# Kernel tuning notes

Hardware: AMD Instinct MI355X
Metric: run time of the kernel (lower is better)

## Reference

```python
import jax, jax.numpy as jnp
import numpy as np

N_NODES = 50000
N_EDGES = 640000
IN_FEATS = 128
HID = 128


def setup_inputs() -> dict:
    key = jax.random.key(0)
    ks = jax.random.split(key, 8)
    x = jax.random.normal(ks[0], (N_NODES, IN_FEATS), dtype=jnp.float32)
    src = jax.random.randint(ks[1], (N_EDGES,), 0, N_NODES, dtype=jnp.int32)
    dst = jax.random.randint(ks[2], (N_EDGES,), 0, N_NODES, dtype=jnp.int32)
    s1 = 1.0 / np.sqrt(IN_FEATS)
    s2 = 1.0 / np.sqrt(HID)
    W1 = jax.random.normal(ks[3], (IN_FEATS, HID), dtype=jnp.float32) * s1
    b1 = jnp.zeros((HID,), dtype=jnp.float32)
    W2 = jax.random.normal(ks[4], (HID, HID), dtype=jnp.float32) * s2
    b2 = jnp.zeros((HID,), dtype=jnp.float32)
    Wr = jax.random.normal(ks[5], (HID, 2), dtype=jnp.float32) * s2
    br = jnp.zeros((2,), dtype=jnp.float32)
    return {"x": x, "src": src, "dst": dst, "W1": W1, "b1": b1,
            "W2": W2, "b2": b2, "Wr": Wr, "br": br}


def _degree_norm(idx, n):
    # D^{-1/2}, with 0 for zero-degree nodes (DGL sets inf -> 0)
    deg = jax.ops.segment_sum(jnp.ones(idx.shape[0], jnp.float32), idx, num_segments=n)
    return jnp.where(deg > 0, jax.lax.rsqrt(jnp.maximum(deg, 1.0)), 0.0)


def _graph_conv(h, W, b, src, dst, norm_out, norm_in, n):
    # DGL GraphConv, norm='both': out = D_in^{-1/2} A D_out^{-1/2} (h W) + b
    hW = (h * norm_out[:, None]) @ W          # [N, hid]
    agg = jax.ops.segment_sum(hW[src], dst, num_segments=n)  # gather+scatter over edges
    return agg * norm_in[:, None] + b


def reference(x, src, dst, W1, b1, W2, b2, Wr, br):
    n = x.shape[0]
    norm_out = _degree_norm(src, n)  # source-side out-degree norm
    norm_in = _degree_norm(dst, n)   # dest-side in-degree norm
    h = jax.nn.relu(_graph_conv(x, W1, b1, src, dst, norm_out, norm_in, n))
    h = jax.nn.relu(_graph_conv(h, W2, b2, src, dst, norm_out, norm_in, n))
    hg = jnp.mean(h, axis=0, keepdims=True)  # [1, hid]
    return hg @ Wr + br                      # [1, 2]
```

## Files before the change

### kernel.cpp

```cpp
#include <hip/hip_runtime.h>
#include <hip/hip_bf16.h>

#define FEAT 128
#define RBITS 13
#define RSIZE 8192
#define NCHUNK 32

typedef __attribute__((ext_vector_type(8))) short short8;
typedef __attribute__((ext_vector_type(4))) short short4v;
typedef __attribute__((ext_vector_type(4))) float f32x4;

__device__ __forceinline__ ushort f2bf(float f) {
    union { float f; unsigned u; } v; v.f = f;
    unsigned u = v.u;
    unsigned r = 0x7fffu + ((u >> 16) & 1u);
    return (ushort)((u + r) >> 16);
}
__device__ __forceinline__ float bf2f(short s) {
    union { unsigned u; float f; } v;
    v.u = ((unsigned)(ushort)s) << 16;
    return v.f;
}

__global__ __launch_bounds__(256)
void hist_kernel(const int* __restrict__ src, const int* __restrict__ dst,
                 unsigned* __restrict__ partial, int E, int CS)
{
    __shared__ unsigned hist[RSIZE];
    const int c = blockIdx.x, p = blockIdx.y, job = blockIdx.z;
    const int* __restrict__ idx = job ? dst : src;
    for (int r = threadIdx.x; r < RSIZE; r += 256) hist[r] = 0;
    __syncthreads();
    const int e0 = c * CS, e1 = min(E, e0 + CS);
    const int eA = e0 + ((e1 - e0) & ~3);
    for (int e = e0 + threadIdx.x * 4; e + 4 <= e1; e += 1024) {
        int4 v = *(const int4*)(idx + e);
        if ((v.x >> RBITS) == p) atomicAdd(&hist[v.x & (RSIZE - 1)], 1u);
        if ((v.y >> RBITS) == p) atomicAdd(&hist[v.y & (RSIZE - 1)], 1u);
        if ((v.z >> RBITS) == p) atomicAdd(&hist[v.z & (RSIZE - 1)], 1u);
        if ((v.w >> RBITS) == p) atomicAdd(&hist[v.w & (RSIZE - 1)], 1u);
    }
    for (int e = eA + threadIdx.x; e < e1; e += 256) {
        int v = idx[e];
        if ((v >> RBITS) == p) atomicAdd(&hist[v & (RSIZE - 1)], 1u);
    }
    __syncthreads();
    unsigned* outp = partial +
        (((size_t)job * gridDim.y + p) * NCHUNK + c) * RSIZE;
    for (int r = threadIdx.x; r < RSIZE; r += 256) outp[r] = hist[r];
}

__global__ __launch_bounds__(256)
void merge_kernel(const unsigned* __restrict__ partialOut, unsigned* __restrict__ partialIn,
                  int* __restrict__ cntIn, float* __restrict__ normOut,
                  float* __restrict__ normIn, int* __restrict__ blockSums, int N)
{
    __shared__ int sh[256];
    const int n = blockIdx.x * 256 + threadIdx.x;
    unsigned off = 0;
    if (n < N) {
        const int p = n >> RBITS, r = n & (RSIZE - 1);
        const size_t base = (size_t)p * NCHUNK * RSIZE + r;
        unsigned so = 0;
#pragma unroll 8
        for (int c = 0; c < NCHUNK; ++c) so += partialOut[base + (size_t)c * RSIZE];
#pragma unroll 8
        for (int c = 0; c < NCHUNK; ++c) {
            size_t i = base + (size_t)c * RSIZE;
            unsigned t = partialIn[i];
            partialIn[i] = off;
            off += t;
        }
        cntIn[n]   = (int)off;
        normIn[n]  = off ? rsqrtf((float)off) : 0.0f;
        normOut[n] = so  ? rsqrtf((float)so)  : 0.0f;
    }
    sh[threadIdx.x] = (int)off;
    __syncthreads();
    for (int o = 128; o > 0; o >>= 1) {
        if (threadIdx.x < o) sh[threadIdx.x] += sh[threadIdx.x + o];
        __syncthreads();
    }
    if (threadIdx.x == 0) blockSums[blockIdx.x] = sh[0];
}

__global__ __launch_bounds__(256)
void rowstart_kernel(const int* __restrict__ cntIn, const int* __restrict__ blockSums,
                     int* __restrict__ rowStart, int N, int NB, int E)
{
    __shared__ int bs[256];
    __shared__ int bse[256];
    __shared__ int sh[256];
    const int t = threadIdx.x;
    int bv = (t < NB) ? blockSums[t] : 0;
    bs[t] = bv;
    __syncthreads();
    for (int off = 1; off < 256; off <<= 1) {
        int u = (t >= off) ? bs[t - off] : 0;
        __syncthreads();
        bs[t] += u;
        __syncthreads();
    }
    bse[t] = bs[t] - bv;
    __syncthreads();

    const int i = blockIdx.x * 256 + t;
    int v = (i < N) ? cntIn[i] : 0;
    sh[t] = v;
    __syncthreads();
    for (int off = 1; off < 256; off <<= 1) {
        int u = (t >= off) ? sh[t - off] : 0;
        __syncthreads();
        sh[t] += u;
        __syncthreads();
    }
    if (i < N) rowStart[i] = bse[blockIdx.x] + sh[t] - v;
    if (blockIdx.x == 0 && t == 0) rowStart[N] = E;
}

__global__ __launch_bounds__(256)
void fill_kernel(const int* __restrict__ src, const int* __restrict__ dst,
                 const int* __restrict__ rowStart, const unsigned* __restrict__ chunkOff,
                 int* __restrict__ csrSrc, int N, int E, int CS)
{
    __shared__ unsigned cursor[RSIZE];
    const int c = blockIdx.x, p = blockIdx.y;
    const unsigned* co = chunkOff + ((size_t)p * NCHUNK + c) * RSIZE;
    for (int r = threadIdx.x; r < RSIZE; r += 256) {
        int n = (p << RBITS) + r;
        cursor[r] = (n < N) ? (unsigned)rowStart[n] + co[r] : 0u;
    }
    __syncthreads();
    const int e0 = c * CS, e1 = min(E, e0 + CS);
    const int eA = e0 + ((e1 - e0) & ~3);
    for (int e = e0 + threadIdx.x * 4; e + 4 <= e1; e += 1024) {
        int4 d = *(const int4*)(dst + e);
        if ((d.x >> RBITS) == p) { unsigned q = atomicAdd(&cursor[d.x & (RSIZE - 1)], 1u); csrSrc[q] = src[e]; }
        if ((d.y >> RBITS) == p) { unsigned q = atomicAdd(&cursor[d.y & (RSIZE - 1)], 1u); csrSrc[q] = src[e + 1]; }
        if ((d.z >> RBITS) == p) { unsigned q = atomicAdd(&cursor[d.z & (RSIZE - 1)], 1u); csrSrc[q] = src[e + 2]; }
        if ((d.w >> RBITS) == p) { unsigned q = atomicAdd(&cursor[d.w & (RSIZE - 1)], 1u); csrSrc[q] = src[e + 3]; }
    }
    for (int e = eA + threadIdx.x; e < e1; e += 256) {
        int d = dst[e];
        if ((d >> RBITS) == p) { unsigned q = atomicAdd(&cursor[d & (RSIZE - 1)], 1u); csrSrc[q] = src[e]; }
    }
}

__global__ __launch_bounds__(256)
void gemm_mfma_kernel(const float* __restrict__ Ain, const float* __restrict__ W,
                      const float* __restrict__ scale, ushort* __restrict__ C,
                      int M, int nStrips)
{
    __shared__ ushort WTAs[128 * 132];
    __shared__ float  sScale[64];
    ushort* WT = WTAs;
    ushort* As = WTAs;

    const int tid  = threadIdx.x;
    const int wv   = tid >> 6;
    const int lane = tid & 63;
    const int rowHalf = wv >> 1;
    const int colHalf = wv & 1;
    const int l15  = lane & 15;
    const int quad = lane >> 4;

    for (int it = 0; it < 16; ++it) {
        int fid = tid + (it << 8);
        int k   = fid >> 5;
        int c4  = (fid & 31) << 2;
        float4 w = *(const float4*)(W + (size_t)k * FEAT + c4);
        WT[(c4 + 0) * 132 + k] = f2bf(w.x);
        WT[(c4 + 1) * 132 + k] = f2bf(w.y);
        WT[(c4 + 2) * 132 + k] = f2bf(w.z);
        WT[(c4 + 3) * 132 + k] = f2bf(w.w);
    }
    __syncthreads();

    short8 bfrag[4][4];
#pragma unroll
    for (int ct = 0; ct < 4; ++ct) {
        int col = colHalf * 64 + ct * 16 + l15;
#pragma unroll
        for (int kst = 0; kst < 4; ++kst) {
            int k = kst * 32 + quad * 8;
            short4v lo = *(const short4v*)&WT[col * 132 + k];
            short4v hi = *(const short4v*)&WT[col * 132 + k + 4];
            bfrag[ct][kst] = __builtin_shufflevector(lo, hi, 0, 1, 2, 3, 4, 5, 6, 7);
        }
    }

    for (int s = blockIdx.x; s < nStrips; s += gridDim.x) {
        const int row0 = s << 6;
        __syncthreads();

#pragma unroll
        for (int it = 0; it < 4; ++it) {
            int fid = tid + (it << 8);
            int r   = fid >> 4;
            int seg = (fid & 15) << 3;
            int grow = row0 + r;
            short4v lo = {0, 0, 0, 0}, hi = {0, 0, 0, 0};
            if (grow < M) {
                const float* pa = Ain + (size_t)grow * FEAT + seg;
                float4 u0 = *(const float4*)(pa);
                float4 u1 = *(const float4*)(pa + 4);
                lo[0] = (short)f2bf(u0.x); lo[1] = (short)f2bf(u0.y);
                lo[2] = (short)f2bf(u0.z); lo[3] = (short)f2bf(u0.w);
                hi[0] = (short)f2bf(u1.x); hi[1] = (short)f2bf(u1.y);
                hi[2] = (short)f2bf(u1.z); hi[3] = (short)f2bf(u1.w);
            }
            *(short4v*)&As[r * 132 + seg]     = lo;
            *(short4v*)&As[r * 132 + seg + 4] = hi;
        }
        if (tid < 64) {
            int grow = row0 + tid;
            sScale[tid] = (grow < M) ? scale[grow] : 0.0f;
        }
        __syncthreads();

        f32x4 acc[2][4] = {};
#pragma unroll
        for (int kst = 0; kst < 4; ++kst) {
            int k = kst * 32 + quad * 8;
            short8 af[2];
#pragma unroll
            for (int rt = 0; rt < 2; ++rt) {
                int row = rowHalf * 32 + rt * 16 + l15;
                short4v lo = *(const short4v*)&As[row * 132 + k];
                short4v hi = *(const short4v*)&As[row * 132 + k + 4];
                af[rt] = __builtin_shufflevector(lo, hi, 0, 1, 2, 3, 4, 5, 6, 7);
            }
#pragma unroll
            for (int rt = 0; rt < 2; ++rt)
#pragma unroll
                for (int ct = 0; ct < 4; ++ct)
                    acc[rt][ct] = __builtin_amdgcn_mfma_f32_16x16x32_bf16(
                        af[rt], bfrag[ct][kst], acc[rt][ct], 0, 0, 0);
        }

#pragma unroll
        for (int rt = 0; rt < 2; ++rt) {
            int rbase = rowHalf * 32 + rt * 16 + quad * 4;
#pragma unroll
            for (int reg = 0; reg < 4; ++reg) {
                int rl = rbase + reg;
                int grow = row0 + rl;
                if (grow < M) {
                    float sc = sScale[rl];
#pragma unroll
                    for (int ct = 0; ct < 4; ++ct) {
                        int col = colHalf * 64 + ct * 16 + l15;
                        C[(size_t)grow * FEAT + col] = f2bf(acc[rt][ct][reg] * sc);
                    }
                }
            }
        }
    }
}

__global__ __launch_bounds__(256)
void fusedA_kernel(const ushort* __restrict__ t1, const int* __restrict__ rowStart,
                   const int* __restrict__ csrSrc, const float* __restrict__ normIn,
                   const float* __restrict__ bias, const float* __restrict__ W,
                   const float* __restrict__ normOut, ushort* __restrict__ t2, int N)
{
    __shared__ ushort WTAs[128 * 132];
    __shared__ float  sScale[64];
    ushort* WT = WTAs;
    ushort* As = WTAs;

    const int tid  = threadIdx.x;
    const int wv   = tid >> 6;
    const int lane = tid & 63;
    const int rowHalf = wv >> 1;
    const int colHalf = wv & 1;
    const int l15  = lane & 15;
    const int quad = lane >> 4;
    const int row0 = blockIdx.x << 6;

    for (int it = 0; it < 16; ++it) {
        int fid = tid + (it << 8);
        int k   = fid >> 5;
        int c4  = (fid & 31) << 2;
        float4 w = *(const float4*)(W + (size_t)k * FEAT + c4);
        WT[(c4 + 0) * 132 + k] = f2bf(w.x);
        WT[(c4 + 1) * 132 + k] = f2bf(w.y);
        WT[(c4 + 2) * 132 + k] = f2bf(w.z);
        WT[(c4 + 3) * 132 + k] = f2bf(w.w);
    }
    if (tid < 64) {
        int grow = row0 + tid;
        sScale[tid] = (grow < N) ? normOut[grow] : 0.0f;
    }
    __syncthreads();

    short8 bfrag[4][4];
#pragma unroll
    for (int ct = 0; ct < 4; ++ct) {
        int col = colHalf * 64 + ct * 16 + l15;
#pragma unroll
        for (int kst = 0; kst < 4; ++kst) {
            int k = kst * 32 + quad * 8;
            short4v lo = *(const short4v*)&WT[col * 132 + k];
            short4v hi = *(const short4v*)&WT[col * 132 + k + 4];
            bfrag[ct][kst] = __builtin_shufflevector(lo, hi, 0, 1, 2, 3, 4, 5, 6, 7);
        }
    }
    __syncthreads();

    {
        const int g    = tid >> 5;
        const int gl   = tid & 31;
        const int h    = gl >> 4;
        const int li   = gl & 15;
        const float4 b0 = *(const float4*)(bias + li * 8);
        const float4 b1 = *(const float4*)(bias + li * 8 + 4);
        for (int i = g; i < 64; i += 8) {
            const int node = row0 + i;
            float a[8] = {0.f, 0.f, 0.f, 0.f, 0.f, 0.f, 0.f, 0.f};
            if (node < N) {
                const int s = rowStart[node];
                const int e = rowStart[node + 1];
                for (int base = s; base < e; base += 32) {
                    const int m = min(32, e - base);
                    int idx = (base + gl < e) ? csrSrc[base + gl] : 0;
                    for (int j0 = 0; j0 < m; j0 += 8) {
                        const int jh = j0 + h;
                        int s0 = __shfl(idx, jh,     32);
                        int s1 = __shfl(idx, jh + 2, 32);
                        int s2 = __shfl(idx, jh + 4, 32);
                        int s3 = __shfl(idx, jh + 6, 32);
                        short8 v0 = {0,0,0,0,0,0,0,0}, v1 = {0,0,0,0,0,0,0,0};
                        short8 v2 = {0,0,0,0,0,0,0,0}, v3 = {0,0,0,0,0,0,0,0};
                        if (jh     < m) v0 = *(const short8*)(t1 + (size_t)s0 * FEAT + li * 8);
                        if (jh + 2 < m) v1 = *(const short8*)(t1 + (size_t)s1 * FEAT + li * 8);
                        if (jh + 4 < m) v2 = *(const short8*)(t1 + (size_t)s2 * FEAT + li * 8);
                        if (jh + 6 < m) v3 = *(const short8*)(t1 + (size_t)s3 * FEAT + li * 8);
#pragma unroll
                        for (int k = 0; k < 8; ++k)
                            a[k] += (bf2f(v0[k]) + bf2f(v1[k])) + (bf2f(v2[k]) + bf2f(v3[k]));
                    }
                }
            }
#pragma unroll
            for (int k = 0; k < 8; ++k)
                a[k] += __shfl_xor(a[k], 16, 32);
            if (h == 0) {
                short8 o = {0,0,0,0,0,0,0,0};
                if (node < N) {
                    float ni = normIn[node];
                    o[0] = (short)f2bf(fmaxf(fmaf(a[0], ni, b0.x), 0.0f));
                    o[1] = (short)f2bf(fmaxf(fmaf(a[1], ni, b0.y), 0.0f));
                    o[2] = (short)f2bf(fmaxf(fmaf(a[2], ni, b0.z), 0.0f));
                    o[3] = (short)f2bf(fmaxf(fmaf(a[3], ni, b0.w), 0.0f));
                    o[4] = (short)f2bf(fmaxf(fmaf(a[4], ni, b1.x), 0.0f));
                    o[5] = (short)f2bf(fmaxf(fmaf(a[5], ni, b1.y), 0.0f));
                    o[6] = (short)f2bf(fmaxf(fmaf(a[6], ni, b1.z), 0.0f));
                    o[7] = (short)f2bf(fmaxf(fmaf(a[7], ni, b1.w), 0.0f));
                }
                *(short8*)&As[i * 132 + li * 8] = o;
            }
        }
    }
    __syncthreads();

    f32x4 acc[2][4] = {};
#pragma unroll
    for (int kst = 0; kst < 4; ++kst) {
        int k = kst * 32 + quad * 8;
        short8 af[2];
#pragma unroll
        for (int rt = 0; rt < 2; ++rt) {
            int row = rowHalf * 32 + rt * 16 + l15;
            short4v lo = *(const short4v*)&As[row * 132 + k];
            short4v hi = *(const short4v*)&As[row * 132 + k + 4];
            af[rt] = __builtin_shufflevector(lo, hi, 0, 1, 2, 3, 4, 5, 6, 7);
        }
#pragma unroll
        for (int rt = 0; rt < 2; ++rt)
#pragma unroll
            for (int ct = 0; ct < 4; ++ct)
                acc[rt][ct] = __builtin_amdgcn_mfma_f32_16x16x32_bf16(
                    af[rt], bfrag[ct][kst], acc[rt][ct], 0, 0, 0);
    }

#pragma unroll
    for (int rt = 0; rt < 2; ++rt) {
        int rbase = rowHalf * 32 + rt * 16 + quad * 4;
#pragma unroll
        for (int reg = 0; reg < 4; ++reg) {
            int rl = rbase + reg;
            int grow = row0 + rl;
            if (grow < N) {
                float sc = sScale[rl];
#pragma unroll
                for (int ct = 0; ct < 4; ++ct) {
                    int col = colHalf * 64 + ct * 16 + l15;
                    t2[(size_t)grow * FEAT + col] = f2bf(acc[rt][ct][reg] * sc);
                }
            }
        }
    }
}

__global__ __launch_bounds__(256)
void fusedB_kernel(const ushort* __restrict__ t2, const int* __restrict__ rowStart,
                   const int* __restrict__ csrSrc, const float* __restrict__ normIn,
                   const float* __restrict__ bias, float* __restrict__ partials, int N)
{
    const int g    = threadIdx.x >> 5;
    const int gl   = threadIdx.x & 31;
    const int h    = gl >> 4;
    const int li   = gl & 15;
    const float4 b0 = *(const float4*)(bias + li * 8);
    const float4 b1 = *(const float4*)(bias + li * 8 + 4);
    const int stride = gridDim.x * 8;

    float racc[8] = {0.f, 0.f, 0.f, 0.f, 0.f, 0.f, 0.f, 0.f};
    for (int node = blockIdx.x * 8 + g; node < N; node += stride) {
        const int s = rowStart[node];
        const int e = rowStart[node + 1];
        float a[8] = {0.f, 0.f, 0.f, 0.f, 0.f, 0.f, 0.f, 0.f};
        for (int base = s; base < e; base += 32) {
            const int m = min(32, e - base);
            int idx = (base + gl < e) ? csrSrc[base + gl] : 0;
            for (int j0 = 0; j0 < m; j0 += 8) {
                const int jh = j0 + h;
                int s0 = __shfl(idx, jh,     32);
                int s1 = __shfl(idx, jh + 2, 32);
                int s2 = __shfl(idx, jh + 4, 32);
                int s3 = __shfl(idx, jh + 6, 32);
                short8 v0 = {0,0,0,0,0,0,0,0}, v1 = {0,0,0,0,0,0,0,0};
                short8 v2 = {0,0,0,0,0,0,0,0}, v3 = {0,0,0,0,0,0,0,0};
                if (jh     < m) v0 = *(const short8*)(t2 + (size_t)s0 * FEAT + li * 8);
                if (jh + 2 < m) v1 = *(const short8*)(t2 + (size_t)s1 * FEAT + li * 8);
                if (jh + 4 < m) v2 = *(const short8*)(t2 + (size_t)s2 * FEAT + li * 8);
                if (jh + 6 < m) v3 = *(const short8*)(t2 + (size_t)s3 * FEAT + li * 8);
#pragma unroll
                for (int k = 0; k < 8; ++k)
                    a[k] += (bf2f(v0[k]) + bf2f(v1[k])) + (bf2f(v2[k]) + bf2f(v3[k]));
            }
        }
#pragma unroll
        for (int k = 0; k < 8; ++k)
            a[k] += __shfl_xor(a[k], 16, 32);
        if (h == 0) {
            float ni = normIn[node];
            racc[0] += fmaxf(fmaf(a[0], ni, b0.x), 0.0f);
            racc[1] += fmaxf(fmaf(a[1], ni, b0.y), 0.0f);
            racc[2] += fmaxf(fmaf(a[2], ni, b0.z), 0.0f);
            racc[3] += fmaxf(fmaf(a[3], ni, b0.w), 0.0f);
            racc[4] += fmaxf(fmaf(a[4], ni, b1.x), 0.0f);
            racc[5] += fmaxf(fmaf(a[5], ni, b1.y), 0.0f);
            racc[6] += fmaxf(fmaf(a[6], ni, b1.z), 0.0f);
            racc[7] += fmaxf(fmaf(a[7], ni, b1.w), 0.0f);
        }
    }

    __shared__ float colsh[8][128];
    if (h == 0) {
#pragma unroll
        for (int k = 0; k < 8; ++k) colsh[g][li * 8 + k] = racc[k];
    }
    __syncthreads();
    if (threadIdx.x < 128) {
        float sum = 0.f;
#pragma unroll
        for (int gg = 0; gg < 8; ++gg) sum += colsh[gg][threadIdx.x];
        partials[(size_t)blockIdx.x * 128 + threadIdx.x] = sum;
    }
}

__global__ __launch_bounds__(1024)
void final_kernel(const float* __restrict__ partials, const float* __restrict__ Wr,
                  const float* __restrict__ br, float* __restrict__ out, float invN, int G)
{
    __shared__ float cs[128];
    __shared__ float s0[128], s1[128];
    if (threadIdx.x < 128) cs[threadIdx.x] = 0.0f;
    __syncthreads();

    const int c4 = (threadIdx.x & 31) << 2;
    const int rg = threadIdx.x >> 5;
    f32x4 acc = {0.f, 0.f, 0.f, 0.f};
    for (int b = rg; b < G; b += 32) {
        f32x4 v = *(const f32x4*)(partials + (size_t)b * 128 + c4);
        acc += v;
    }
    atomicAdd(&cs[c4 + 0], acc[0]);
    atomicAdd(&cs[c4 + 1], acc[1]);
    atomicAdd(&cs[c4 + 2], acc[2]);
    atomicAdd(&cs[c4 + 3], acc[3]);
    __syncthreads();

    const int j = threadIdx.x;
    if (j < 128) {
        float hg = cs[j] * invN;
        s0[j] = hg * Wr[2 * j + 0];
        s1[j] = hg * Wr[2 * j + 1];
    }
    __syncthreads();
    for (int off = 64; off > 0; off >>= 1) {
        if (j < off) { s0[j] += s0[j + off]; s1[j] += s1[j + off]; }
        __syncthreads();
    }
    if (j == 0) {
        out[0] = s0[0] + br[0];
        out[1] = s1[0] + br[1];
    }
}

extern "C" void kernel_launch(void* const* d_in, const int* in_sizes, int n_in,
                              void* d_out, int out_size, void* d_ws, size_t ws_size,
                              hipStream_t stream)
{
    const float* x   = (const float*)d_in[0];
    const int*   src = (const int*)d_in[1];
    const int*   dst = (const int*)d_in[2];
    const float* W1  = (const float*)d_in[3];
    const float* b1  = (const float*)d_in[4];
    const float* W2  = (const float*)d_in[5];
    const float* b2  = (const float*)d_in[6];
    const float* Wr  = (const float*)d_in[7];
    const float* br  = (const float*)d_in[8];
    float* out = (float*)d_out;

    const int N = in_sizes[0] / FEAT;
    const int E = in_sizes[1];
    const int NP = ((N + 255) / 256) * 256;
    const int NB = (N + 255) / 256;
    const int P  = (N + RSIZE - 1) / RSIZE;
    const int CS = (((E + NCHUNK - 1) / NCHUNK) + 3) & ~3;
    const int GB = 1024;

    char* p = (char*)d_ws;
    unsigned* partial = (unsigned*)p;    p += (size_t)2 * P * NCHUNK * RSIZE * 4;
    int*    blockSums = (int*)p;         p += 256 * 4;
    int*    cntIn     = (int*)p;         p += (size_t)NP * 4;
    float*  normOut   = (float*)p;       p += (size_t)NP * 4;
    float*  normIn    = (float*)p;       p += (size_t)NP * 4;
    int*    rowStart  = (int*)p;         p += (size_t)(NP + 64) * 4;
    int*    csrSrc    = (int*)p;         p += (size_t)E * 4;
    float*  partials  = (float*)p;       p += (size_t)GB * 128 * 4;
    ushort* bufT1     = (ushort*)p;      p += (size_t)N * FEAT * 2;
    ushort* bufT2     = (ushort*)p;      p += (size_t)N * FEAT * 2;

    unsigned* partialOut = partial;
    unsigned* partialIn  = partial + (size_t)P * NCHUNK * RSIZE;

    hist_kernel<<<dim3(NCHUNK, P, 2), 256, 0, stream>>>(src, dst, partial, E, CS);
    merge_kernel<<<NB, 256, 0, stream>>>(partialOut, partialIn, cntIn, normOut, normIn, blockSums, N);
    rowstart_kernel<<<NB, 256, 0, stream>>>(cntIn, blockSums, rowStart, N, NB, E);
    fill_kernel<<<dim3(NCHUNK, P), 256, 0, stream>>>(src, dst, rowStart, partialIn, csrSrc, N, E, CS);

    const int nStrips = (N + 63) / 64;

    gemm_mfma_kernel<<<nStrips, 256, 0, stream>>>(x, W1, normOut, bufT1, N, nStrips);

    fusedA_kernel<<<nStrips, 256, 0, stream>>>(bufT1, rowStart, csrSrc, normIn, b1, W2, normOut, bufT2, N);

    fusedB_kernel<<<GB, 256, 0, stream>>>(bufT2, rowStart, csrSrc, normIn, b2, partials, N);

    final_kernel<<<1, 1024, 0, stream>>>(partials, Wr, br, out, 1.0f / (float)N, GB);
}
```

Before: 234.7 us.

## Use 512-thread blocks and half-size LDS tile in GEMM and fused aggregation kernels

Both the layer-1 GEMM and the fused aggregate+GEMM kernel now run with 8 waves per block instead of 4. Each wave covers a 32-column quarter of the output, so it holds fewer B fragments and accumulators. The shared transposed-weight tile is cut to 64 columns and loaded in two passes, which halves LDS per block and should allow more resident blocks and better latency hiding for the gather. The cost is an extra barrier pass during weight staging and more waves sharing each block's work.

After: 220.4 us. 6.1% less time.

```diff
diff --git a/kernel.cpp b/kernel.cpp
--- a/kernel.cpp
+++ b/kernel.cpp
@@ -146,12 +146,12 @@
     }
 }
 
-__global__ __launch_bounds__(256)
+__global__ __launch_bounds__(512)
 void gemm_mfma_kernel(const float* __restrict__ Ain, const float* __restrict__ W,
                       const float* __restrict__ scale, ushort* __restrict__ C,
                       int M, int nStrips)
 {
-    __shared__ ushort WTAs[128 * 132];
+    __shared__ ushort WTAs[64 * 132];
     __shared__ float  sScale[64];
     ushort* WT = WTAs;
     ushort* As = WTAs;
@@ -159,33 +159,39 @@
     const int tid  = threadIdx.x;
     const int wv   = tid >> 6;
     const int lane = tid & 63;
-    const int rowHalf = wv >> 1;
-    const int colHalf = wv & 1;
+    const int rowHalf = wv >> 2;
+    const int colQ = wv & 3;
     const int l15  = lane & 15;
     const int quad = lane >> 4;
 
-    for (int it = 0; it < 16; ++it) {
-        int fid = tid + (it << 8);
-        int k   = fid >> 5;
-        int c4  = (fid & 31) << 2;
-        float4 w = *(const float4*)(W + (size_t)k * FEAT + c4);
-        WT[(c4 + 0) * 132 + k] = f2bf(w.x);
-        WT[(c4 + 1) * 132 + k] = f2bf(w.y);
-        WT[(c4 + 2) * 132 + k] = f2bf(w.z);
-        WT[(c4 + 3) * 132 + k] = f2bf(w.w);
-    }
-    __syncthreads();
-
-    short8 bfrag[4][4];
-#pragma unroll
-    for (int ct = 0; ct < 4; ++ct) {
-        int col = colHalf * 64 + ct * 16 + l15;
-#pragma unroll
-        for (int kst = 0; kst < 4; ++kst) {
-            int k = kst * 32 + quad * 8;
-            short4v lo = *(const short4v*)&WT[col * 132 + k];
-            short4v hi = *(const short4v*)&WT[col * 132 + k + 4];
-            bfrag[ct][kst] = __builtin_shufflevector(lo, hi, 0, 1, 2, 3, 4, 5, 6, 7);
+    short8 bfrag[2][4];
+#pragma unroll
+    for (int hh = 0; hh < 2; ++hh) {
+        if (hh) __syncthreads();
+        for (int it = 0; it < 4; ++it) {
+            int fid = tid + (it << 9);
+            int k   = fid >> 4;
+            int cl  = (fid & 15) << 2;
+            float4 w = *(const float4*)(W + (size_t)k * FEAT + hh * 64 + cl);
+            WT[(cl + 0) * 132 + k] = f2bf(w.x);
+            WT[(cl + 1) * 132 + k] = f2bf(w.y);
+            WT[(cl + 2) * 132 + k] = f2bf(w.z);
+            WT[(cl + 3) * 132 + k] = f2bf(w.w);
+        }
+        __syncthreads();
+        if (((wv >> 1) & 1) == hh) {
+            int cq = wv & 1;
+#pragma unroll
+            for (int ct = 0; ct < 2; ++ct) {
+                int col = cq * 32 + ct * 16 + l15;
+#pragma unroll
+                for (int kst = 0; kst < 4; ++kst) {
+                    int k = kst * 32 + quad * 8;
+                    short4v lo = *(const short4v*)&WT[col * 132 + k];
+                    short4v hi = *(const short4v*)&WT[col * 132 + k + 4];
+                    bfrag[ct][kst] = __builtin_shufflevector(lo, hi, 0, 1, 2, 3, 4, 5, 6, 7);
+                }
+            }
         }
     }
 
@@ -194,8 +200,8 @@
         __syncthreads();
 
 #pragma unroll
-        for (int it = 0; it < 4; ++it) {
-            int fid = tid + (it << 8);
+        for (int it = 0; it < 2; ++it) {
+            int fid = tid + (it << 9);
             int r   = fid >> 4;
             int seg = (fid & 15) << 3;
             int grow = row0 + r;
@@ -218,7 +224,7 @@
         }
         __syncthreads();
 
-        f32x4 acc[2][4] = {};
+        f32x4 acc[2][2] = {};
 #pragma unroll
         for (int kst = 0; kst < 4; ++kst) {
             int k = kst * 32 + quad * 8;
@@ -233,7 +239,7 @@
 #pragma unroll
             for (int rt = 0; rt < 2; ++rt)
 #pragma unroll
-                for (int ct = 0; ct < 4; ++ct)
+                for (int ct = 0; ct < 2; ++ct)
                     acc[rt][ct] = __builtin_amdgcn_mfma_f32_16x16x32_bf16(
                         af[rt], bfrag[ct][kst], acc[rt][ct], 0, 0, 0);
         }
@@ -248,8 +254,8 @@
                 if (grow < M) {
                     float sc = sScale[rl];
 #pragma unroll
-                    for (int ct = 0; ct < 4; ++ct) {
-                        int col = colHalf * 64 + ct * 16 + l15;
+                    for (int ct = 0; ct < 2; ++ct) {
+                        int col = colQ * 32 + ct * 16 + l15;
                         C[(size_t)grow * FEAT + col] = f2bf(acc[rt][ct][reg] * sc);
                     }
                 }
@@ -258,13 +264,13 @@
     }
 }
 
-__global__ __launch_bounds__(256)
+__global__ __launch_bounds__(512)
 void fusedA_kernel(const ushort* __restrict__ t1, const int* __restrict__ rowStart,
                    const int* __restrict__ csrSrc, const float* __restrict__ normIn,
                    const float* __restrict__ bias, const float* __restrict__ W,
                    const float* __restrict__ normOut, ushort* __restrict__ t2, int N)
 {
-    __shared__ ushort WTAs[128 * 132];
+    __shared__ ushort WTAs[64 * 132];
     __shared__ float  sScale[64];
     ushort* WT = WTAs;
     ushort* As = WTAs;
@@ -272,39 +278,45 @@
     const int tid  = threadIdx.x;
     const int wv   = tid >> 6;
     const int lane = tid & 63;
-    const int rowHalf = wv >> 1;
-    const int colHalf = wv & 1;
+    const int rowHalf = wv >> 2;
+    const int colQ = wv & 3;
     const int l15  = lane & 15;
     const int quad = lane >> 4;
     const int row0 = blockIdx.x << 6;
 
-    for (int it = 0; it < 16; ++it) {
-        int fid = tid + (it << 8);
-        int k   = fid >> 5;
-        int c4  = (fid & 31) << 2;
-        float4 w = *(const float4*)(W + (size_t)k * FEAT + c4);
-        WT[(c4 + 0) * 132 + k] = f2bf(w.x);
-        WT[(c4 + 1) * 132 + k] = f2bf(w.y);
-        WT[(c4 + 2) * 132 + k] = f2bf(w.z);
-        WT[(c4 + 3) * 132 + k] = f2bf(w.w);
+    short8 bfrag[2][4];
+#pragma unroll
+    for (int hh = 0; hh < 2; ++hh) {
+        if (hh) __syncthreads();
+        for (int it = 0; it < 4; ++it) {
+            int fid = tid + (it << 9);
+            int k   = fid >> 4;
+            int cl  = (fid & 15) << 2;
+            float4 w = *(const float4*)(W + (size_t)k * FEAT + hh * 64 + cl);
+            WT[(cl + 0) * 132 + k] = f2bf(w.x);
+            WT[(cl + 1) * 132 + k] = f2bf(w.y);
+            WT[(cl + 2) * 132 + k] = f2bf(w.z);
+            WT[(cl + 3) * 132 + k] = f2bf(w.w);
+        }
+        __syncthreads();
+        if (((wv >> 1) & 1) == hh) {
+            int cq = wv & 1;
+#pragma unroll
+            for (int ct = 0; ct < 2; ++ct) {
+                int col = cq * 32 + ct * 16 + l15;
+#pragma unroll
+                for (int kst = 0; kst < 4; ++kst) {
+                    int k = kst * 32 + quad * 8;
+                    short4v lo = *(const short4v*)&WT[col * 132 + k];
+                    short4v hi = *(const short4v*)&WT[col * 132 + k + 4];
+                    bfrag[ct][kst] = __builtin_shufflevector(lo, hi, 0, 1, 2, 3, 4, 5, 6, 7);
+                }
+            }
+        }
     }
     if (tid < 64) {
         int grow = row0 + tid;
         sScale[tid] = (grow < N) ? normOut[grow] : 0.0f;
-    }
-    __syncthreads();
-
-    short8 bfrag[4][4];
-#pragma unroll
-    for (int ct = 0; ct < 4; ++ct) {
-        int col = colHalf * 64 + ct * 16 + l15;
-#pragma unroll
-        for (int kst = 0; kst < 4; ++kst) {
-            int k = kst * 32 + quad * 8;
-            short4v lo = *(const short4v*)&WT[col * 132 + k];
-            short4v hi = *(const short4v*)&WT[col * 132 + k + 4];
-            bfrag[ct][kst] = __builtin_shufflevector(lo, hi, 0, 1, 2, 3, 4, 5, 6, 7);
-        }
     }
     __syncthreads();
 
@@ -315,7 +327,7 @@
         const int li   = gl & 15;
         const float4 b0 = *(const float4*)(bias + li * 8);
         const float4 b1 = *(const float4*)(bias + li * 8 + 4);
-        for (int i = g; i < 64; i += 8) {
+        for (int i = g; i < 64; i += 16) {
             const int node = row0 + i;
             float a[8] = {0.f, 0.f, 0.f, 0.f, 0.f, 0.f, 0.f, 0.f};
             if (node < N) {
@@ -364,7 +376,7 @@
     }
     __syncthreads();
 
-    f32x4 acc[2][4] = {};
+    f32x4 acc[2][2] = {};
 #pragma unroll
     for (int kst = 0; kst < 4; ++kst) {
         int k = kst * 32 + quad * 8;
@@ -379,7 +391,7 @@
 #pragma unroll
         for (int rt = 0; rt < 2; ++rt)
 #pragma unroll
-            for (int ct = 0; ct < 4; ++ct)
+            for (int ct = 0; ct < 2; ++ct)
                 acc[rt][ct] = __builtin_amdgcn_mfma_f32_16x16x32_bf16(
                     af[rt], bfrag[ct][kst], acc[rt][ct], 0, 0, 0);
     }
@@ -394,8 +406,8 @@
             if (grow < N) {
                 float sc = sScale[rl];
 #pragma unroll
-                for (int ct = 0; ct < 4; ++ct) {
-                    int col = colHalf * 64 + ct * 16 + l15;
+                for (int ct = 0; ct < 2; ++ct) {
+                    int col = colQ * 32 + ct * 16 + l15;
                     t2[(size_t)grow * FEAT + col] = f2bf(acc[rt][ct][reg] * sc);
                 }
             }
@@ -555,9 +567,9 @@
 
     const int nStrips = (N + 63) / 64;
 
-    gemm_mfma_kernel<<<nStrips, 256, 0, stream>>>(x, W1, normOut, bufT1, N, nStrips);
-
-    fusedA_kernel<<<nStrips, 256, 0, stream>>>(bufT1, rowStart, csrSrc, normIn, b1, W2, normOut, bufT2, N);
+    gemm_mfma_kernel<<<nStrips, 512, 0, stream>>>(x, W1, normOut, bufT1, N, nStrips);
+
+    fusedA_kernel<<<nStrips, 512, 0, stream>>>(bufT1, rowStart, csrSrc, normIn, b1, W2, normOut, bufT2, N);
 
     fusedB_kernel<<<GB, 256, 0, stream>>>(bufT2, rowStart, csrSrc, normIn, b2, partials, N);
 
```
